# Kernel optimization log

Hardware: AMD Instinct MI355X
Metric: run time of the kernel (lower is better)

## Reference

```python
import jax, jax.numpy as jnp
import numpy as np

C = 256
G = 32            # GroupNorm groups = min(32, C)
DQK = C // 8      # q/k channel dim
EPS = 1e-5


def setup_inputs() -> dict:
    key = jax.random.key(0)
    ks = jax.random.split(key, 10)
    B, H, W = 4, 64, 64
    s = 0.02
    return {
        "x": jax.random.normal(ks[0], (B, C, H, W), dtype=jnp.float32),
        "gamma": jnp.ones((C,), jnp.float32),
        "beta": jnp.zeros((C,), jnp.float32),
        "wq": jax.random.normal(ks[1], (DQK, C), jnp.float32) * s,
        "bq": jnp.zeros((DQK,), jnp.float32),
        "wk": jax.random.normal(ks[2], (DQK, C), jnp.float32) * s,
        "bk": jnp.zeros((DQK,), jnp.float32),
        "wv": jax.random.normal(ks[3], (C, C), jnp.float32) * s,
        "bv": jnp.zeros((C,), jnp.float32),
        "wp": jax.random.normal(ks[4], (C, C), jnp.float32) * s,
        "bp": jnpp if False else jnp.zeros((C,), jnp.float32),
    }


def reference(x, gamma, beta, wq, bq, wk, bk, wv, bv, wp, bp):
    B, Cc, H, W = x.shape
    N = H * W
    # GroupNorm(32, C), affine
    h = x.reshape(B, G, Cc // G, H, W)
    mu = h.mean(axis=(2, 3, 4), keepdims=True)
    var = h.var(axis=(2, 3, 4), keepdims=True)
    h = (h - mu) * jax.lax.rsqrt(var + EPS)
    h = h.reshape(B, Cc, N) * gamma[:, None] + beta[:, None]
    # 1x1 convs == per-token linear maps over channels
    q = jnp.einsum('dc,bcn->bnd', wq, h) + bq            # [B, N, DQK]
    k = jnp.einsum('dc,bcn->bdn', wk, h) + bk[:, None]   # [B, DQK, N]
    v = jnp.einsum('ec,bcn->ben', wv, h) + bv[:, None]   # [B, C, N]
    scale = DQK ** (-0.5)
    attn = jax.nn.softmax(jnp.einsum('bnd,bdm->bnm', q, k) * scale, axis=-1)
    out = jnp.einsum('bnm,bem->ben', attn, v)            # [B, C, N]
    proj = jnp.einsum('fe,ben->bfn', wp, out) + bp[:, None]
    return x + proj.reshape(B, Cc, H, W)
```

## Files before the change

### kernel.cpp

```cpp
#include <hip/hip_runtime.h>
#include <hip/hip_bf16.h>

#define NB 4
#define CD 256
#define NT 4096
#define DQ 32

typedef __attribute__((ext_vector_type(8))) __bf16 bf16x8;
typedef __attribute__((ext_vector_type(16))) float float16v;
typedef __attribute__((ext_vector_type(4))) unsigned int uint4v;
typedef __attribute__((ext_vector_type(2))) unsigned int uint2v;

#if __has_builtin(__builtin_amdgcn_exp2f)
#define EXP2(x) __builtin_amdgcn_exp2f(x)
#else
#define EXP2(x) exp2f(x)
#endif

__device__ inline unsigned short f2bf(float f) {
  unsigned u = __float_as_uint(f);
  u += 0x7fffu + ((u >> 16) & 1u);
  return (unsigned short)(u >> 16);
}

#define BARRIER() asm volatile("s_waitcnt lgkmcnt(0)\n\ts_barrier" ::: "memory")

__global__ __launch_bounds__(1024) void gn_fused(
    const float* __restrict__ x, const float* __restrict__ gamma,
    const float* __restrict__ beta, const float* __restrict__ wq,
    const float* __restrict__ wk, const float* __restrict__ wv,
    const float* __restrict__ wp, const float* __restrict__ bq,
    const float* __restrict__ bk, const float* __restrict__ bv,
    unsigned short* __restrict__ h, unsigned short* __restrict__ wqkv,
    unsigned short* __restrict__ wpb, float* __restrict__ bias) {
  int bx = blockIdx.x;
  int tid = threadIdx.x;
  if (bx < 128) {
    int b = bx >> 5, g = bx & 31, c0 = g * 8;
    const float4* xp = (const float4*)(x + (size_t)bx * 32768);
    float va[32];
    float s = 0.f, ss = 0.f;
#pragma unroll
    for (int i = 0; i < 8; i++) {
      float4 t4 = xp[i * 1024 + tid];
      va[4 * i + 0] = t4.x;
      va[4 * i + 1] = t4.y;
      va[4 * i + 2] = t4.z;
      va[4 * i + 3] = t4.w;
      s += t4.x + t4.y + t4.z + t4.w;
      ss += t4.x * t4.x + t4.y * t4.y + t4.z * t4.z + t4.w * t4.w;
    }
#pragma unroll
    for (int off = 32; off >= 1; off >>= 1) {
      s += __shfl_xor(s, off);
      ss += __shfl_xor(ss, off);
    }
    __shared__ float red[32];
    int wid = tid >> 6;
    if ((tid & 63) == 0) {
      red[wid] = s;
      red[16 + wid] = ss;
    }
    __syncthreads();
    float S = 0.f, SS = 0.f;
#pragma unroll
    for (int i = 0; i < 16; i++) {
      S += red[i];
      SS += red[16 + i];
    }
    float mu = S * (1.f / 32768.f);
    float rstd = rsqrtf(SS * (1.f / 32768.f) - mu * mu + 1e-5f);
    float gam[8], bet[8];
#pragma unroll
    for (int i = 0; i < 8; i++) {
      gam[i] = gamma[c0 + i] * rstd;
      bet[i] = beta[c0 + i] - mu * gamma[c0 + i] * rstd;
    }
    unsigned short* hb = h + (size_t)b * NT * CD + c0;
#pragma unroll
    for (int j = 0; j < 4; j++) {
      unsigned short hv[8];
#pragma unroll
      for (int i = 0; i < 8; i++) {
        hv[i] = f2bf(va[4 * i + j] * gam[i] + bet[i]);
      }
      *(uint4v*)(hb + (size_t)(4 * tid + j) * CD) = *(uint4v*)hv;
    }
  } else {
    const float scale2 = 0.2550348909867343f;
    int i = (bx - 128) * 1024 + tid;
    if (i < 320 * 256) {
      int j = i >> 8, c = i & 255;
      float v;
      if (j < 32) v = wq[j * 256 + c] * scale2;
      else if (j < 64) v = wk[(j - 32) * 256 + c];
      else v = wv[(j - 64) * 256 + c];
      wqkv[i] = f2bf(v);
    } else if (i < 320 * 256 + 256 * 256) {
      int k = i - 320 * 256;
      wpb[k] = f2bf(wp[k]);
    } else if (i < 320 * 256 + 256 * 256 + 320) {
      int j = i - (320 * 256 + 256 * 256);
      float v;
      if (j < 32) v = bq[j] * scale2;
      else if (j < 64) v = bk[j - 32];
      else v = bv[j - 64];
      bias[j] = v;
    }
  }
}

__global__ __launch_bounds__(256) void qkv_gemm(
    const unsigned short* __restrict__ A, const unsigned short* __restrict__ H,
    const float* __restrict__ bias, unsigned short* __restrict__ qk,
    unsigned short* __restrict__ v) {
  int nt = blockIdx.x, mt = blockIdx.y, b = blockIdx.z;
  int tid = threadIdx.x, lane = tid & 63;
  int w = tid >> 6, mi = w & 1, nq = w >> 1;
  int l31 = lane & 31, hh = lane >> 5;
  int n0 = nt * 64;
  int m_base = mt * 64 + 32 * mi;

  __shared__ unsigned short Hs[64 * 260];
  const unsigned short* Hb = H + (size_t)b * NT * CD;
#pragma unroll
  for (int u = 0; u < 8; u++) {
    int idx = u * 256 + tid;
    int row = idx >> 5, col = (idx & 31) * 8;
    *(uint4v*)&Hs[row * 260 + col] =
        *(const uint4v*)&Hb[(size_t)(n0 + row) * CD + col];
  }
  __syncthreads();

  const unsigned short* Arow = A + (size_t)(m_base + l31) * 256 + 8 * hh;
  const unsigned short* Brow = &Hs[(nq * 32 + l31) * 260 + 8 * hh];
  float16v acc;
#pragma unroll
  for (int r = 0; r < 16; r++) acc[r] = 0.f;
#pragma unroll
  for (int s = 0; s < 16; s++) {
    bf16x8 af = *(const bf16x8*)(Arow + 16 * s);
    bf16x8 bf = *(const bf16x8*)(Brow + 16 * s);
    acc = __builtin_amdgcn_mfma_f32_32x32x16_bf16(af, bf, acc, 0, 0, 0);
  }
  int n = n0 + nq * 32 + l31;
  int itg = n >> 6, sp = (n >> 4) & 3;
  int lsn = ((n >> 3) & 1) * 32;
  int el = n & 7;
#pragma unroll
  for (int r = 0; r < 16; r++) {
    int j = m_base + (r & 3) + 8 * (r >> 2) + 4 * hh;
    float val = acc[r] + bias[j];
    if (j < 64) {
      qk[((size_t)b * NT + n) * 64 + j] = f2bf(val);
    } else {
      int e = j - 64;
      int et = e >> 5;
      v[((((size_t)b * 64 + itg) * 8 + et) * 4 + sp) * 512 + (lsn + (e & 31)) * 8 +
        el] = f2bf(val);
    }
  }
}

#define K_STAGE(PCUR)                                                         \
  if (tid >= 256) {                                                           \
    *(uint4v*)&Ks[(((PCUR) + 1) & 1) * 2304 + skr * 36 + skc] = kreg;         \
    int pk_ = (PCUR) + 2 <= 31 ? (PCUR) + 2 : 31;                             \
    kreg =                                                                    \
        *(const uint4v*)&qkb[(size_t)(mbase + pk_ * 64 + skr) * 64 + 32 + skc]; \
  }

#define QK_STEP(PCUR)                                                         \
  if (w < 4) {                                                                \
    float16v st;                                                              \
    _Pragma("unroll") for (int r = 0; r < 16; r++) st[r] = 0.f;               \
    __builtin_amdgcn_s_setprio(1);                                            \
    _Pragma("unroll") for (int s = 0; s < 2; s++) {                           \
      bf16x8 af = *(const bf16x8*)&Ks[((PCUR) & 1) * 2304 +                   \
                                      (32 * ks2 + l31) * 36 + 16 * s + 8 * hh]; \
      st = __builtin_amdgcn_mfma_f32_32x32x16_bf16(af, qfr[s], st, 0, 0, 0);  \
    }                                                                         \
    __builtin_amdgcn_s_setprio(0);                                            \
    _Pragma("unroll") for (int rq = 0; rq < 4; rq++) {                        \
      float e0 = EXP2(st[4 * rq + 0]);                                        \
      float e1 = EXP2(st[4 * rq + 1]);                                        \
      float e2 = EXP2(st[4 * rq + 2]);                                        \
      float e3 = EXP2(st[4 * rq + 3]);                                        \
      lsum += (e0 + e1) + (e2 + e3);                                          \
      uint2v pw;                                                              \
      pw[0] = __builtin_amdgcn_perm(__float_as_uint(e1), __float_as_uint(e0), \
                                    0x07060302u);                             \
      pw[1] = __builtin_amdgcn_perm(__float_as_uint(e3), __float_as_uint(e2), \
                                    0x07060302u);                             \
      *(uint2v*)&Pbuf[((PCUR) & 1) * 4352 + (qs * 32 + l31) * 68 + 8 * rq +   \
                      4 * hh + 32 * ks2] = pw;                                \
    }                                                                         \
  }

#define PV_STEP(PPREV, CURV)                                                  \
  {                                                                           \
    __builtin_amdgcn_s_setprio(1);                                            \
    _Pragma("unroll") for (int sp = 0; sp < 4; sp++) {                        \
      bf16x8 a0 = *(const bf16x8*)&Pbuf[((PPREV) & 1) * 4352 + l31 * 68 +     \
                                        16 * sp + 8 * hh];                    \
      bf16x8 a1 = *(const bf16x8*)&Pbuf[((PPREV) & 1) * 4352 +                \
                                        (32 + l31) * 68 + 16 * sp + 8 * hh];  \
      acc[0] = __builtin_amdgcn_mfma_f32_32x32x16_bf16(a0, CURV[sp], acc[0],  \
                                                       0, 0, 0);              \
      acc[1] = __builtin_amdgcn_mfma_f32_32x32x16_bf16(a1, CURV[sp], acc[1],  \
                                                       0, 0, 0);              \
    }                                                                         \
    __builtin_amdgcn_s_setprio(0);                                            \
  }

#define V_LOAD(DST, ITX)                                                      \
  {                                                                           \
    const unsigned short* vp_ = vbase + (size_t)(ITX)*16384;                  \
    _Pragma("unroll") for (int u = 0; u < 4; u++)                             \
        DST[u] = *(const bf16x8*)(vp_ + u * 512);                             \
  }

__global__ __launch_bounds__(512, 4) void attn_fused(
    const unsigned short* __restrict__ qk, const unsigned short* __restrict__ Vp,
    unsigned short* __restrict__ Pa, unsigned short* __restrict__ Pb,
    float* __restrict__ lp4) {
  int L = blockIdx.x;
  int xv = L & 7;
  int b = xv >> 1;
  int kh = xv & 1;
  int n0 = (L >> 3) * 64;
  int tid = threadIdx.x, lane = tid & 63, w = tid >> 6;
  int l31 = lane & 31, hh = lane >> 5;
  int qs = w & 1, ks2 = (w >> 1) & 1;

  __shared__ unsigned short Ks[2 * 2304];
  __shared__ unsigned short Pbuf[2 * 4352];

  const unsigned short* qkb = qk + (size_t)b * NT * 64;
  const unsigned short* vit = Vp + ((size_t)b * 64 + kh * 32) * 16384;
  const unsigned short* vbase = vit + (size_t)w * 4 * 512 + lane * 8;

  bf16x8 qfr[2];
  if (w < 4) {
    int n_g = n0 + 32 * qs + l31;
    qfr[0] = *(const bf16x8*)&qkb[(size_t)n_g * 64 + 8 * hh];
    qfr[1] = *(const bf16x8*)&qkb[(size_t)n_g * 64 + 8 * hh + 16];
  }

  int tK = tid - 256;
  int skr = tK >> 2, skc = (tK & 3) * 8;
  int mbase = kh * 2048;
  uint4v kreg;

  float16v acc[2];
#pragma unroll
  for (int q2 = 0; q2 < 2; q2++)
#pragma unroll
    for (int r = 0; r < 16; r++) acc[q2][r] = 0.f;
  float lsum = 0.f;

  bf16x8 vA[4], vB[4];
  V_LOAD(vA, 0);
  if (tid >= 256) {
    kreg = *(const uint4v*)&qkb[(size_t)(mbase + skr) * 64 + 32 + skc];
    *(uint4v*)&Ks[skr * 36 + skc] = kreg;
    kreg = *(const uint4v*)&qkb[(size_t)(mbase + 64 + skr) * 64 + 32 + skc];
  }
  BARRIER();

  K_STAGE(0);
  QK_STEP(0);
  V_LOAD(vB, 1);
  BARRIER();

  for (int p = 1; p < 31; p += 2) {
    K_STAGE(p);
    QK_STEP(p);
    PV_STEP(p - 1, vA);
    V_LOAD(vA, p + 1);
    BARRIER();
    K_STAGE(p + 1);
    QK_STEP(p + 1);
    PV_STEP(p, vB);
    V_LOAD(vB, p + 2);
    BARRIER();
  }
  QK_STEP(31);
  PV_STEP(30, vA);
  BARRIER();
  PV_STEP(31, vB);

  if (w < 4) {
    lsum += __shfl_xor(lsum, 32);
    if (hh == 0) {
      lp4[(size_t)((kh * 2 + ks2) * NB + b) * NT + n0 + 32 * qs + l31] = lsum;
    }
  }

  unsigned short* Pout = (kh ? Pb : Pa) + (size_t)b * NT * CD;
#pragma unroll
  for (int r = 0; r < 16; r++) {
    int nl = (r & 3) + 8 * (r >> 2) + 4 * hh;
    Pout[(size_t)(n0 + nl) * CD + 32 * w + l31] = f2bf(acc[0][r]);
    Pout[(size_t)(n0 + 32 + nl) * CD + 32 * w + l31] = f2bf(acc[1][r]);
  }
}

__global__ __launch_bounds__(256) void proj_gemm(
    const unsigned short* __restrict__ Wp, const unsigned short* __restrict__ Pa,
    const unsigned short* __restrict__ Pb, const float* __restrict__ lp4,
    const float* __restrict__ bp, const float* __restrict__ x,
    float* __restrict__ out) {
  int nt = blockIdx.x, mh = blockIdx.y, b = blockIdx.z;
  int tid = threadIdx.x, lane = tid & 63;
  int w = tid >> 6;
  int l31 = lane & 31, hh = lane >> 5;
  int n0 = nt * 64;

  __shared__ unsigned short Bs[64 * 260];
  int r0 = tid >> 5, colb = (tid & 31) * 8;
#pragma unroll
  for (int u = 0; u < 8; u++) {
    int row = r0 + 8 * u;
    float lA = 0.f;
#pragma unroll
    for (int s4 = 0; s4 < 4; s4++)
      lA += lp4[(size_t)(s4 * NB + b) * NT + n0 + row];
    float inv = 1.f / lA;
    size_t goff = ((size_t)b * NT + n0 + row) * CD + colb;
    uint4v ua = *(const uint4v*)(Pa + goff);
    uint4v ub = *(const uint4v*)(Pb + goff);
    uint4v rr;
#pragma unroll
    for (int j = 0; j < 4; j++) {
      float lo = __uint_as_float(ua[j] << 16) + __uint_as_float(ub[j] << 16);
      float hi = __uint_as_float(ua[j] & 0xffff0000u) +
                 __uint_as_float(ub[j] & 0xffff0000u);
      lo *= inv;
      hi *= inv;
      rr[j] = __builtin_amdgcn_perm(__float_as_uint(hi), __float_as_uint(lo),
                                    0x07060302u);
    }
    *(uint4v*)&Bs[row * 260 + colb] = rr;
  }
  __syncthreads();

  int m_base = mh * 128 + w * 32;
  const unsigned short* Arow = Wp + (size_t)(m_base + l31) * 256 + 8 * hh;
  const unsigned short* b0p = &Bs[l31 * 260 + 8 * hh];
  const unsigned short* b1p = &Bs[(32 + l31) * 260 + 8 * hh];
  float16v acc0, acc1;
#pragma unroll
  for (int r = 0; r < 16; r++) { acc0[r] = 0.f; acc1[r] = 0.f; }
#pragma unroll
  for (int s = 0; s < 16; s++) {
    bf16x8 af = *(const bf16x8*)(Arow + 16 * s);
    bf16x8 bf0 = *(const bf16x8*)(b0p + 16 * s);
    bf16x8 bf1 = *(const bf16x8*)(b1p + 16 * s);
    acc0 = __builtin_amdgcn_mfma_f32_32x32x16_bf16(af, bf0, acc0, 0, 0, 0);
    acc1 = __builtin_amdgcn_mfma_f32_32x32x16_bf16(af, bf1, acc1, 0, 0, 0);
  }
#pragma unroll
  for (int nq = 0; nq < 2; nq++) {
    int n = n0 + nq * 32 + l31;
#pragma unroll
    for (int r = 0; r < 16; r++) {
      int f = m_base + (r & 3) + 8 * (r >> 2) + 4 * hh;
      size_t idx = ((size_t)b * CD + f) * NT + n;
      out[idx] = x[idx] + (nq ? acc1[r] : acc0[r]) + bp[f];
    }
  }
}

extern "C" void kernel_launch(void* const* d_in, const int* in_sizes, int n_in,
                              void* d_out, int out_size, void* d_ws,
                              size_t ws_size, hipStream_t stream) {
  (void)in_sizes; (void)n_in; (void)out_size; (void)ws_size;
  const float* x = (const float*)d_in[0];
  const float* gamma = (const float*)d_in[1];
  const float* beta = (const float*)d_in[2];
  const float* wq = (const float*)d_in[3];
  const float* bq = (const float*)d_in[4];
  const float* wk = (const float*)d_in[5];
  const float* bk = (const float*)d_in[6];
  const float* wv = (const float*)d_in[7];
  const float* bv = (const float*)d_in[8];
  const float* wp = (const float*)d_in[9];
  const float* bp = (const float*)d_in[10];
  float* out = (float*)d_out;

  char* ws = (char*)d_ws;
  unsigned short* h_ws = (unsigned short*)ws;
  unsigned short* qk_ws = (unsigned short*)(ws + 8388608);
  unsigned short* v_ws = (unsigned short*)(ws + 10485760);
  unsigned short* o_ws = (unsigned short*)(ws + 18874368);
  unsigned short* wqkv_b = (unsigned short*)(ws + 27262976);
  unsigned short* wp_b = (unsigned short*)(ws + 27426816);
  float* bias_q = (float*)(ws + 27557888);
  float* lp4 = (float*)(ws + 27563264);

  gn_fused<<<273, 1024, 0, stream>>>(x, gamma, beta, wq, wk, wv, wp, bq, bk,
                                     bv, h_ws, wqkv_b, wp_b, bias_q);
  dim3 gq(64, 5, NB);
  qkv_gemm<<<gq, 256, 0, stream>>>(wqkv_b, h_ws, bias_q, qk_ws, v_ws);
  attn_fused<<<512, 512, 0, stream>>>(qk_ws, v_ws, h_ws, o_ws, lp4);
  dim3 gp(64, 2, NB);
  proj_gemm<<<gp, 256, 0, stream>>>(wp_b, h_ws, o_ws, lp4, bp, x, out);
}
```

Before: 189.9 us.

## Fuse GroupNorm apply into QKV GEMM and double-step attention pipeline

The stats kernel now only computes per-channel scale/shift, and the QKV kernel reads x directly and normalizes it into LDS before the GEMM. This removes the round trip through the normalized bf16 h buffer. Each QKV block now computes all 320 output rows for its 64 tokens with a 2x2 MFMA tile per wave, so x is read once per token tile. The attention loop processes two K/V tiles per barrier, with four-way LDS buffers, halving the number of barriers at the cost of more LDS and registers.

```diff
diff --git a/kernel.cpp b/kernel.cpp
--- a/kernel.cpp
+++ b/kernel.cpp
@@ -25,28 +25,24 @@
 
 #define BARRIER() asm volatile("s_waitcnt lgkmcnt(0)\n\ts_barrier" ::: "memory")
 
-__global__ __launch_bounds__(1024) void gn_fused(
+__global__ __launch_bounds__(1024) void stats_pack(
     const float* __restrict__ x, const float* __restrict__ gamma,
     const float* __restrict__ beta, const float* __restrict__ wq,
     const float* __restrict__ wk, const float* __restrict__ wv,
     const float* __restrict__ wp, const float* __restrict__ bq,
     const float* __restrict__ bk, const float* __restrict__ bv,
-    unsigned short* __restrict__ h, unsigned short* __restrict__ wqkv,
-    unsigned short* __restrict__ wpb, float* __restrict__ bias) {
+    float* __restrict__ sc, float* __restrict__ sh,
+    unsigned short* __restrict__ wqkv, unsigned short* __restrict__ wpb,
+    float* __restrict__ bias) {
   int bx = blockIdx.x;
   int tid = threadIdx.x;
   if (bx < 128) {
-    int b = bx >> 5, g = bx & 31, c0 = g * 8;
+    int b = bx >> 5, g = bx & 31;
     const float4* xp = (const float4*)(x + (size_t)bx * 32768);
-    float va[32];
     float s = 0.f, ss = 0.f;
 #pragma unroll
     for (int i = 0; i < 8; i++) {
       float4 t4 = xp[i * 1024 + tid];
-      va[4 * i + 0] = t4.x;
-      va[4 * i + 1] = t4.y;
-      va[4 * i + 2] = t4.z;
-      va[4 * i + 3] = t4.w;
       s += t4.x + t4.y + t4.z + t4.w;
       ss += t4.x * t4.x + t4.y * t4.y + t4.z * t4.z + t4.w * t4.w;
     }
@@ -62,29 +58,19 @@
       red[16 + wid] = ss;
     }
     __syncthreads();
-    float S = 0.f, SS = 0.f;
-#pragma unroll
-    for (int i = 0; i < 16; i++) {
-      S += red[i];
-      SS += red[16 + i];
-    }
-    float mu = S * (1.f / 32768.f);
-    float rstd = rsqrtf(SS * (1.f / 32768.f) - mu * mu + 1e-5f);
-    float gam[8], bet[8];
-#pragma unroll
-    for (int i = 0; i < 8; i++) {
-      gam[i] = gamma[c0 + i] * rstd;
-      bet[i] = beta[c0 + i] - mu * gamma[c0 + i] * rstd;
-    }
-    unsigned short* hb = h + (size_t)b * NT * CD + c0;
-#pragma unroll
-    for (int j = 0; j < 4; j++) {
-      unsigned short hv[8];
-#pragma unroll
-      for (int i = 0; i < 8; i++) {
-        hv[i] = f2bf(va[4 * i + j] * gam[i] + bet[i]);
+    if (tid < 8) {
+      float S = 0.f, SS = 0.f;
+#pragma unroll
+      for (int i = 0; i < 16; i++) {
+        S += red[i];
+        SS += red[16 + i];
       }
-      *(uint4v*)(hb + (size_t)(4 * tid + j) * CD) = *(uint4v*)hv;
+      float mu = S * (1.f / 32768.f);
+      float rstd = rsqrtf(SS * (1.f / 32768.f) - mu * mu + 1e-5f);
+      int c = g * 8 + tid;
+      float gm = gamma[c];
+      sc[b * CD + c] = gm * rstd;
+      sh[b * CD + c] = beta[c] - mu * gm * rstd;
     }
   } else {
     const float scale2 = 0.2550348909867343f;
@@ -110,74 +96,108 @@
   }
 }
 
-__global__ __launch_bounds__(256) void qkv_gemm(
-    const unsigned short* __restrict__ A, const unsigned short* __restrict__ H,
+__global__ __launch_bounds__(512) void qkv_norm(
+    const float* __restrict__ x, const float* __restrict__ sc,
+    const float* __restrict__ sh, const unsigned short* __restrict__ A,
     const float* __restrict__ bias, unsigned short* __restrict__ qk,
     unsigned short* __restrict__ v) {
-  int nt = blockIdx.x, mt = blockIdx.y, b = blockIdx.z;
-  int tid = threadIdx.x, lane = tid & 63;
-  int w = tid >> 6, mi = w & 1, nq = w >> 1;
+  int nt = blockIdx.x, b = blockIdx.y;
+  int tid = threadIdx.x, lane = tid & 63, w = tid >> 6;
   int l31 = lane & 31, hh = lane >> 5;
   int n0 = nt * 64;
-  int m_base = mt * 64 + 32 * mi;
-
-  __shared__ unsigned short Hs[64 * 260];
-  const unsigned short* Hb = H + (size_t)b * NT * CD;
-#pragma unroll
-  for (int u = 0; u < 8; u++) {
-    int idx = u * 256 + tid;
-    int row = idx >> 5, col = (idx & 31) * 8;
-    *(uint4v*)&Hs[row * 260 + col] =
-        *(const uint4v*)&Hb[(size_t)(n0 + row) * CD + col];
+
+  __shared__ unsigned short Hs[64 * 262];
+  const float* xb = x + (size_t)b * CD * NT + n0;
+  const float* scb = sc + b * CD;
+  const float* shb = sh + b * CD;
+#pragma unroll
+  for (int u = 0; u < 4; u++) {
+    int c0 = (w + 8 * u) * 8;
+    float4 s0 = *(const float4*)(scb + c0);
+    float4 s1 = *(const float4*)(scb + c0 + 4);
+    float4 h0 = *(const float4*)(shb + c0);
+    float4 h1 = *(const float4*)(shb + c0 + 4);
+    float scv[8] = {s0.x, s0.y, s0.z, s0.w, s1.x, s1.y, s1.z, s1.w};
+    float shv[8] = {h0.x, h0.y, h0.z, h0.w, h1.x, h1.y, h1.z, h1.w};
+    unsigned short hv[8];
+#pragma unroll
+    for (int j = 0; j < 8; j++) {
+      float val = xb[(size_t)(c0 + j) * NT + lane];
+      hv[j] = f2bf(val * scv[j] + shv[j]);
+    }
+    *(uint4v*)&Hs[lane * 262 + c0] = *(uint4v*)hv;
   }
   __syncthreads();
 
-  const unsigned short* Arow = A + (size_t)(m_base + l31) * 256 + 8 * hh;
-  const unsigned short* Brow = &Hs[(nq * 32 + l31) * 260 + 8 * hh];
-  float16v acc;
-#pragma unroll
-  for (int r = 0; r < 16; r++) acc[r] = 0.f;
-#pragma unroll
-  for (int s = 0; s < 16; s++) {
-    bf16x8 af = *(const bf16x8*)(Arow + 16 * s);
-    bf16x8 bf = *(const bf16x8*)(Brow + 16 * s);
-    acc = __builtin_amdgcn_mfma_f32_32x32x16_bf16(af, bf, acc, 0, 0, 0);
-  }
-  int n = n0 + nq * 32 + l31;
-  int itg = n >> 6, sp = (n >> 4) & 3;
-  int lsn = ((n >> 3) & 1) * 32;
-  int el = n & 7;
-#pragma unroll
-  for (int r = 0; r < 16; r++) {
-    int j = m_base + (r & 3) + 8 * (r >> 2) + 4 * hh;
-    float val = acc[r] + bias[j];
-    if (j < 64) {
-      qk[((size_t)b * NT + n) * 64 + j] = f2bf(val);
-    } else {
-      int e = j - 64;
-      int et = e >> 5;
-      v[((((size_t)b * 64 + itg) * 8 + et) * 4 + sp) * 512 + (lsn + (e & 31)) * 8 +
-        el] = f2bf(val);
-    }
-  }
-}
-
-#define K_STAGE(PCUR)                                                         \
+  if (w < 5) {
+    int m_base = w * 64;
+    const unsigned short* Ar0 = A + (size_t)(m_base + l31) * 256 + 8 * hh;
+    const unsigned short* Ar1 = Ar0 + (size_t)32 * 256;
+    const unsigned short* B0 = &Hs[l31 * 262 + 8 * hh];
+    const unsigned short* B1 = &Hs[(32 + l31) * 262 + 8 * hh];
+    float16v a00, a01, a10, a11;
+#pragma unroll
+    for (int r = 0; r < 16; r++) {
+      a00[r] = 0.f; a01[r] = 0.f; a10[r] = 0.f; a11[r] = 0.f;
+    }
+#pragma unroll
+    for (int s = 0; s < 16; s++) {
+      bf16x8 af0 = *(const bf16x8*)(Ar0 + 16 * s);
+      bf16x8 af1 = *(const bf16x8*)(Ar1 + 16 * s);
+      bf16x8 bf0 = *(const bf16x8*)(B0 + 16 * s);
+      bf16x8 bf1 = *(const bf16x8*)(B1 + 16 * s);
+      a00 = __builtin_amdgcn_mfma_f32_32x32x16_bf16(af0, bf0, a00, 0, 0, 0);
+      a01 = __builtin_amdgcn_mfma_f32_32x32x16_bf16(af0, bf1, a01, 0, 0, 0);
+      a10 = __builtin_amdgcn_mfma_f32_32x32x16_bf16(af1, bf0, a10, 0, 0, 0);
+      a11 = __builtin_amdgcn_mfma_f32_32x32x16_bf16(af1, bf1, a11, 0, 0, 0);
+    }
+#pragma unroll
+    for (int mi = 0; mi < 2; mi++) {
+#pragma unroll
+      for (int nq = 0; nq < 2; nq++) {
+        int n = n0 + nq * 32 + l31;
+        int itg = n >> 6, sp = (n >> 4) & 3;
+        int lsn = ((n >> 3) & 1) * 32;
+        int el = n & 7;
+#pragma unroll
+        for (int r = 0; r < 16; r++) {
+          int j = m_base + 32 * mi + (r & 3) + 8 * (r >> 2) + 4 * hh;
+          float val = (mi ? (nq ? a11[r] : a10[r]) : (nq ? a01[r] : a00[r])) +
+                      bias[j];
+          if (j < 64) {
+            qk[((size_t)b * NT + n) * 64 + j] = f2bf(val);
+          } else {
+            int e = j - 64;
+            int et = e >> 5;
+            v[((((size_t)b * 64 + itg) * 8 + et) * 4 + sp) * 512 +
+              (lsn + (e & 31)) * 8 + el] = f2bf(val);
+          }
+        }
+      }
+    }
+  }
+}
+
+#define K_STAGE2(TNEXT, KSW)                                                  \
   if (tid >= 256) {                                                           \
-    *(uint4v*)&Ks[(((PCUR) + 1) & 1) * 2304 + skr * 36 + skc] = kreg;         \
-    int pk_ = (PCUR) + 2 <= 31 ? (PCUR) + 2 : 31;                             \
-    kreg =                                                                    \
-        *(const uint4v*)&qkb[(size_t)(mbase + pk_ * 64 + skr) * 64 + 32 + skc]; \
-  }
-
-#define QK_STEP(PCUR)                                                         \
+    *(uint4v*)&Ks[(KSW) * 2304 + skr * 36 + skc] = kregA;                     \
+    *(uint4v*)&Ks[((KSW) + 1) * 2304 + skr * 36 + skc] = kregB;               \
+    int ta_ = (TNEXT) > 31 ? 31 : (TNEXT);                                    \
+    int tb_ = (TNEXT) + 1 > 31 ? 31 : (TNEXT) + 1;                            \
+    kregA =                                                                   \
+        *(const uint4v*)&qkb[(size_t)(mbase + ta_ * 64 + skr) * 64 + 32 + skc]; \
+    kregB =                                                                   \
+        *(const uint4v*)&qkb[(size_t)(mbase + tb_ * 64 + skr) * 64 + 32 + skc]; \
+  }
+
+#define QK_ONE(KSB, PBB)                                                      \
   if (w < 4) {                                                                \
     float16v st;                                                              \
     _Pragma("unroll") for (int r = 0; r < 16; r++) st[r] = 0.f;               \
     __builtin_amdgcn_s_setprio(1);                                            \
     _Pragma("unroll") for (int s = 0; s < 2; s++) {                           \
-      bf16x8 af = *(const bf16x8*)&Ks[((PCUR) & 1) * 2304 +                   \
-                                      (32 * ks2 + l31) * 36 + 16 * s + 8 * hh]; \
+      bf16x8 af = *(const bf16x8*)&Ks[(KSB) * 2304 + (32 * ks2 + l31) * 36 +  \
+                                      16 * s + 8 * hh];                       \
       st = __builtin_amdgcn_mfma_f32_32x32x16_bf16(af, qfr[s], st, 0, 0, 0);  \
     }                                                                         \
     __builtin_amdgcn_s_setprio(0);                                            \
@@ -192,32 +212,35 @@
                                     0x07060302u);                             \
       pw[1] = __builtin_amdgcn_perm(__float_as_uint(e3), __float_as_uint(e2), \
                                     0x07060302u);                             \
-      *(uint2v*)&Pbuf[((PCUR) & 1) * 4352 + (qs * 32 + l31) * 68 + 8 * rq +   \
-                      4 * hh + 32 * ks2] = pw;                                \
+      *(uint2v*)&Pbuf[(PBB) * 4352 + (qs * 32 + l31) * 68 + 8 * rq + 4 * hh + \
+                      32 * ks2] = pw;                                         \
     }                                                                         \
   }
 
-#define PV_STEP(PPREV, CURV)                                                  \
+#define PV_ONE(PBB, VS)                                                       \
   {                                                                           \
     __builtin_amdgcn_s_setprio(1);                                            \
     _Pragma("unroll") for (int sp = 0; sp < 4; sp++) {                        \
-      bf16x8 a0 = *(const bf16x8*)&Pbuf[((PPREV) & 1) * 4352 + l31 * 68 +     \
+      bf16x8 a0 =                                                             \
+          *(const bf16x8*)&Pbuf[(PBB) * 4352 + l31 * 68 + 16 * sp + 8 * hh];  \
+      bf16x8 a1 = *(const bf16x8*)&Pbuf[(PBB) * 4352 + (32 + l31) * 68 +      \
                                         16 * sp + 8 * hh];                    \
-      bf16x8 a1 = *(const bf16x8*)&Pbuf[((PPREV) & 1) * 4352 +                \
-                                        (32 + l31) * 68 + 16 * sp + 8 * hh];  \
-      acc[0] = __builtin_amdgcn_mfma_f32_32x32x16_bf16(a0, CURV[sp], acc[0],  \
-                                                       0, 0, 0);              \
-      acc[1] = __builtin_amdgcn_mfma_f32_32x32x16_bf16(a1, CURV[sp], acc[1],  \
-                                                       0, 0, 0);              \
+      acc[0] =                                                                \
+          __builtin_amdgcn_mfma_f32_32x32x16_bf16(a0, VS[sp], acc[0], 0, 0, 0); \
+      acc[1] =                                                                \
+          __builtin_amdgcn_mfma_f32_32x32x16_bf16(a1, VS[sp], acc[1], 0, 0, 0); \
     }                                                                         \
     __builtin_amdgcn_s_setprio(0);                                            \
   }
 
-#define V_LOAD(DST, ITX)                                                      \
+#define V_LOAD2(T)                                                            \
   {                                                                           \
-    const unsigned short* vp_ = vbase + (size_t)(ITX)*16384;                  \
-    _Pragma("unroll") for (int u = 0; u < 4; u++)                             \
-        DST[u] = *(const bf16x8*)(vp_ + u * 512);                             \
+    const unsigned short* vp0_ = vbase + (size_t)(T)*16384;                   \
+    const unsigned short* vp1_ = vbase + (size_t)((T) + 1) * 16384;           \
+    _Pragma("unroll") for (int u = 0; u < 4; u++) {                           \
+      vS0[u] = *(const bf16x8*)(vp0_ + u * 512);                              \
+      vS1[u] = *(const bf16x8*)(vp1_ + u * 512);                              \
+    }                                                                         \
   }
 
 __global__ __launch_bounds__(512, 4) void attn_fused(
@@ -233,8 +256,8 @@
   int l31 = lane & 31, hh = lane >> 5;
   int qs = w & 1, ks2 = (w >> 1) & 1;
 
-  __shared__ unsigned short Ks[2 * 2304];
-  __shared__ unsigned short Pbuf[2 * 4352];
+  __shared__ unsigned short Ks[4 * 2304];
+  __shared__ unsigned short Pbuf[4 * 4352];
 
   const unsigned short* qkb = qk + (size_t)b * NT * 64;
   const unsigned short* vit = Vp + ((size_t)b * 64 + kh * 32) * 16384;
@@ -250,7 +273,7 @@
   int tK = tid - 256;
   int skr = tK >> 2, skc = (tK & 3) * 8;
   int mbase = kh * 2048;
-  uint4v kreg;
+  uint4v kregA, kregB;
 
   float16v acc[2];
 #pragma unroll
@@ -259,36 +282,48 @@
     for (int r = 0; r < 16; r++) acc[q2][r] = 0.f;
   float lsum = 0.f;
 
-  bf16x8 vA[4], vB[4];
-  V_LOAD(vA, 0);
+  bf16x8 vS0[4], vS1[4];
   if (tid >= 256) {
-    kreg = *(const uint4v*)&qkb[(size_t)(mbase + skr) * 64 + 32 + skc];
-    *(uint4v*)&Ks[skr * 36 + skc] = kreg;
-    kreg = *(const uint4v*)&qkb[(size_t)(mbase + 64 + skr) * 64 + 32 + skc];
+    kregA = *(const uint4v*)&qkb[(size_t)(mbase + skr) * 64 + 32 + skc];
+    kregB = *(const uint4v*)&qkb[(size_t)(mbase + 64 + skr) * 64 + 32 + skc];
+    *(uint4v*)&Ks[skr * 36 + skc] = kregA;
+    *(uint4v*)&Ks[2304 + skr * 36 + skc] = kregB;
+    kregA = *(const uint4v*)&qkb[(size_t)(mbase + 128 + skr) * 64 + 32 + skc];
+    kregB = *(const uint4v*)&qkb[(size_t)(mbase + 192 + skr) * 64 + 32 + skc];
   }
   BARRIER();
 
-  K_STAGE(0);
-  QK_STEP(0);
-  V_LOAD(vB, 1);
+  K_STAGE2(4, 2);
+  QK_ONE(0, 0);
+  QK_ONE(1, 1);
+  V_LOAD2(0);
   BARRIER();
 
-  for (int p = 1; p < 31; p += 2) {
-    K_STAGE(p);
-    QK_STEP(p);
-    PV_STEP(p - 1, vA);
-    V_LOAD(vA, p + 1);
+  for (int p = 1; p < 15; p += 2) {
+    K_STAGE2(2 * p + 4, 0);
+    QK_ONE(2, 2);
+    QK_ONE(3, 3);
+    PV_ONE(0, vS0);
+    PV_ONE(1, vS1);
+    V_LOAD2(2 * p);
     BARRIER();
-    K_STAGE(p + 1);
-    QK_STEP(p + 1);
-    PV_STEP(p, vB);
-    V_LOAD(vB, p + 2);
+    K_STAGE2(2 * p + 6, 2);
+    QK_ONE(0, 0);
+    QK_ONE(1, 1);
+    PV_ONE(2, vS0);
+    PV_ONE(3, vS1);
+    V_LOAD2(2 * p + 2);
     BARRIER();
   }
-  QK_STEP(31);
-  PV_STEP(30, vA);
+  K_STAGE2(34, 0);
+  QK_ONE(2, 2);
+  QK_ONE(3, 3);
+  PV_ONE(0, vS0);
+  PV_ONE(1, vS1);
+  V_LOAD2(30);
   BARRIER();
-  PV_STEP(31, vB);
+  PV_ONE(2, vS0);
+  PV_ONE(3, vS1);
 
   if (w < 4) {
     lsum += __shfl_xor(lsum, 32);
@@ -390,7 +425,7 @@
   float* out = (float*)d_out;
 
   char* ws = (char*)d_ws;
-  unsigned short* h_ws = (unsigned short*)ws;
+  unsigned short* pa_ws = (unsigned short*)ws;
   unsigned short* qk_ws = (unsigned short*)(ws + 8388608);
   unsigned short* v_ws = (unsigned short*)(ws + 10485760);
   unsigned short* o_ws = (unsigned short*)(ws + 18874368);
@@ -398,12 +433,15 @@
   unsigned short* wp_b = (unsigned short*)(ws + 27426816);
   float* bias_q = (float*)(ws + 27557888);
   float* lp4 = (float*)(ws + 27563264);
-
-  gn_fused<<<273, 1024, 0, stream>>>(x, gamma, beta, wq, wk, wv, wp, bq, bk,
-                                     bv, h_ws, wqkv_b, wp_b, bias_q);
-  dim3 gq(64, 5, NB);
-  qkv_gemm<<<gq, 256, 0, stream>>>(wqkv_b, h_ws, bias_q, qk_ws, v_ws);
-  attn_fused<<<512, 512, 0, stream>>>(qk_ws, v_ws, h_ws, o_ws, lp4);
+  float* sc_ws = (float*)(ws + 27825408);
+  float* sh_ws = (float*)(ws + 27829504);
+
+  stats_pack<<<273, 1024, 0, stream>>>(x, gamma, beta, wq, wk, wv, wp, bq, bk,
+                                       bv, sc_ws, sh_ws, wqkv_b, wp_b, bias_q);
+  dim3 gq(64, NB);
+  qkv_norm<<<gq, 512, 0, stream>>>(x, sc_ws, sh_ws, wqkv_b, bias_q, qk_ws,
+                                   v_ws);
+  attn_fused<<<512, 512, 0, stream>>>(qk_ws, v_ws, pa_ws, o_ws, lp4);
   dim3 gp(64, 2, NB);
-  proj_gemm<<<gp, 256, 0, stream>>>(wp_b, h_ws, o_ws, lp4, bp, x, out);
-}
+  proj_gemm<<<gp, 256, 0, stream>>>(wp_b, pa_ws, o_ws, lp4, bp, x, out);
+}
```

Result: faster. 174.8 us (-7.9%).
